# Kernel tuning notes

Hardware: AMD Instinct MI355X
Metric: run time of the kernel (lower is better)

The kernel has to match this reference:

```python
import jax, jax.numpy as jnp
import numpy as np

B, S, H, E, V = 16, 512, 1024, 256, 50257


def setup_inputs() -> dict:
    key = jax.random.key(0)
    ks = jax.random.split(key, 16)
    sc = 0.02
    return {
        "x": jax.random.randint(ks[0], (B, 1), 0, V),
        "dec_hs": jax.random.normal(ks[1], (1, B, H), jnp.float32),
        "enc_output": jax.random.normal(ks[2], (S, B, H), jnp.float32),
        "emb": jax.random.normal(ks[3], (V, E), jnp.float32) * sc,
        "w1_W": jax.random.normal(ks[4], (H, H), jnp.float32) * sc,
        "w1_b": jnp.zeros((H,), jnp.float32),
        "w2_W": jax.random.normal(ks[5], (H, H), jnp.float32) * sc,
        "w2_b": jnp.zeros((H,), jnp.float32),
        "va_W": jax.random.normal(ks[6], (1, H), jnp.float32) * sc,
        "va_b": jnp.zeros((1,), jnp.float32),
        "W_ih": jax.random.normal(ks[7], (3 * H, E + H), jnp.float32) * sc,
        "W_hh": jax.random.normal(ks[8], (3 * H, H), jnp.float32) * sc,
        "b_ih": jnp.zeros((3 * H,), jnp.float32),
        "b_hh": jnp.zeros((3 * H,), jnp.float32),
        "out_W": jax.random.normal(ks[9], (V, H), jnp.float32) * sc,
        "out_b": jnp.zeros((V,), jnp.float32),
    }


def reference(x, dec_hs, enc_output, emb, w1_W, w1_b, w2_W, w2_b, va_W, va_b,
              W_ih, W_hh, b_ih, b_hh, out_W, out_b):
    # --- Bahdanau attention ---
    # dec_hs: [1,B,H], enc_output: [S,B,H]
    dec_proj = dec_hs @ w1_W.T + w1_b           # [1,B,H]
    enc_proj = enc_output @ w2_W.T + w2_b       # [S,B,H]
    score = jnp.tanh(dec_proj + enc_proj) @ va_W.T + va_b  # [S,B,1]
    score = jnp.transpose(score, (1, 0, 2))     # [B,S,1]
    attn = jax.nn.softmax(score, axis=1)        # [B,S,1]
    context = jnp.sum(attn * jnp.transpose(enc_output, (1, 0, 2)), axis=1)  # [B,H]

    # --- embedding + concat (context first, as in torch.cat([ctx, emb])) ---
    e = emb[x[:, 0]]                            # [B,E]
    gru_in = jnp.concatenate([context, e], axis=-1)  # [B,H+E]

    # --- GRU single step; NOTE: original calls self.GRU(inp) without dec_hs,
    # so the initial hidden state is zeros (faithful to the source). ---
    h0 = jnp.zeros((gru_in.shape[0], w1_W.shape[0]), gru_in.dtype)  # [B,H]
    gi = gru_in @ W_ih.T + b_ih                 # [B,3H]
    gh = h0 @ W_hh.T + b_hh                     # [B,3H]
    i_r, i_z, i_n = jnp.split(gi, 3, axis=-1)
    h_r, h_z, h_n = jnp.split(gh, 3, axis=-1)
    r = jax.nn.sigmoid(i_r + h_r)
    z = jax.nn.sigmoid(i_z + h_z)
    n = jnp.tanh(i_n + r * h_n)
    h = (1.0 - z) * n + z * h0                  # [B,H]

    fc_out = h @ out_W.T + out_b                # [B,V]
    new_dec_hs = h[None]                        # [1,B,H]
    return fc_out, new_dec_hs, attn
```

## Files before the change

### kernel.cpp

```cpp
#include <hip/hip_runtime.h>
#include <hip/hip_bf16.h>

typedef unsigned short u16;
typedef __attribute__((ext_vector_type(4))) float f32x4;
typedef __attribute__((ext_vector_type(8))) __bf16 bf16x8;
typedef __attribute__((ext_vector_type(8))) unsigned short ushort8;

#define Bb 16
#define Ss 512
#define Hh 1024
#define Ee 256
#define Vv 50257
#define Mm 8192

#define WS_ENC_BF   0
#define WS_W2_BF    16777216
#define WS_DPW      18874368
#define WS_SCORE    18939904
#define WS_GRUIN    18972672
#define WS_GI       19054592

__device__ __forceinline__ u16 f2bf(float f) {
  unsigned u = __float_as_uint(f);
  return (u16)((u + 0x7FFFu + ((u >> 16) & 1u)) >> 16);
}

__device__ __forceinline__ void gl2lds16(const void* g, void* l) {
  __builtin_amdgcn_global_load_lds((__attribute__((address_space(1))) void*)g,
                                   (__attribute__((address_space(3))) void*)l,
                                   16, 0, 0);
}

__global__ __launch_bounds__(256) void k_cvt2(const float* __restrict__ enc, u16* __restrict__ encb,
                                              const float* __restrict__ w2, u16* __restrict__ w2b) {
  int i = blockIdx.x * 256 + threadIdx.x;
  const float* src; u16* dst; int j;
  if (i < 1048576) { src = enc; dst = encb; j = i; }
  else             { src = w2;  dst = w2b;  j = i - 1048576; }
  const float4* s4 = (const float4*)src;
  float4 a = s4[j * 2], c = s4[j * 2 + 1];
  ushort8 o;
  o[0] = f2bf(a.x); o[1] = f2bf(a.y); o[2] = f2bf(a.z); o[3] = f2bf(a.w);
  o[4] = f2bf(c.x); o[5] = f2bf(c.y); o[6] = f2bf(c.z); o[7] = f2bf(c.w);
  *(ushort8*)(dst + j * 8) = o;
}

__global__ __launch_bounds__(256) void k_prep(const float* __restrict__ dec_hs, const float* __restrict__ w1_W,
                                              const float* __restrict__ w1_b, const float* __restrict__ w2_b,
                                              const float* __restrict__ va_b, const int* __restrict__ x,
                                              const float* __restrict__ emb, float* __restrict__ dpw,
                                              float* __restrict__ score, float* __restrict__ gru_in) {
  const int n = blockIdx.x, t = threadIdx.x;
  float acc[16];
#pragma unroll
  for (int b = 0; b < 16; ++b) acc[b] = 0.f;
#pragma unroll
  for (int i = 0; i < 4; ++i) {
    int k = t + i * 256;
    float w = w1_W[n * Hh + k];
#pragma unroll
    for (int b = 0; b < 16; ++b) acc[b] = fmaf(w, dec_hs[b * Hh + k], acc[b]);
  }
#pragma unroll
  for (int m = 1; m < 64; m <<= 1)
#pragma unroll
    for (int b = 0; b < 16; ++b) acc[b] += __shfl_xor(acc[b], m, 64);
  __shared__ float red[4][16];
  int wave = t >> 6, lane = t & 63;
  if (lane == 0)
#pragma unroll
    for (int b = 0; b < 16; ++b) red[wave][b] = acc[b];
  __syncthreads();
  if (t < 16)
    dpw[t * Hh + n] = red[0][t] + red[1][t] + red[2][t] + red[3][t] + w1_b[n] + w2_b[n];
  int fid = n * 256 + t;
  if (fid < 16384) { int b = fid >> 10, k = fid & 1023; gru_in[b * 1280 + k] = 0.f; }
  int sid = fid - 16384;
  if (sid >= 0 && sid < Mm) score[sid] = va_b[0];
  int eid = fid - 24576;
  if (eid >= 0 && eid < 4096) { int b = eid >> 8, j = eid & 255; gru_in[b * 1280 + 1024 + j] = emb[x[b] * Ee + j]; }
}

__global__ __launch_bounds__(256) void k_gemm_score(const u16* __restrict__ A, const u16* __restrict__ Bm,
                                                    const float* __restrict__ dpw, const float* __restrict__ vaW,
                                                    float* __restrict__ score) {
  __shared__ __align__(16) u16 Al[4096];
  __shared__ __align__(16) u16 Bl[4096];
  const int tid = threadIdx.x;
  const int wave = tid >> 6, lane = tid & 63;
  const int quad = lane >> 4, l16 = lane & 15;
  const int m0 = blockIdx.x * 128, n0 = blockIdx.y * 128;
  const int wm = (wave & 1) * 64, wn = (wave >> 1) * 64;

  f32x4 acc[4][4];
#pragma unroll
  for (int i = 0; i < 4; ++i)
#pragma unroll
    for (int j = 0; j < 4; ++j) acc[i][j] = (f32x4){0.f, 0.f, 0.f, 0.f};

  const u16* gA = A + (m0 + (tid >> 2)) * 1024 + (tid & 3) * 8;
  const u16* gB = Bm + (n0 + (tid >> 2)) * 1024 + (tid & 3) * 8;
  u16* lA0 = &Al[(wave * 64) * 8];
  u16* lA1 = &Al[(256 + wave * 64) * 8];
  u16* lB0 = &Bl[(wave * 64) * 8];
  u16* lB1 = &Bl[(256 + wave * 64) * 8];

  for (int kt = 0; kt < 1024; kt += 32) {
    __syncthreads();
    gl2lds16(gA + kt, lA0);
    gl2lds16(gA + 64 * 1024 + kt, lA1);
    gl2lds16(gB + kt, lB0);
    gl2lds16(gB + 64 * 1024 + kt, lB1);
    __syncthreads();
    bf16x8 af[4], bfr[4];
#pragma unroll
    for (int i = 0; i < 4; ++i) {
      af[i]  = *(const bf16x8*)&Al[(wm + i * 16 + l16) * 32 + quad * 8];
      bfr[i] = *(const bf16x8*)&Bl[(wn + i * 16 + l16) * 32 + quad * 8];
    }
#pragma unroll
    for (int i = 0; i < 4; ++i)
#pragma unroll
      for (int j = 0; j < 4; ++j)
        acc[i][j] = __builtin_amdgcn_mfma_f32_16x16x32_bf16(af[i], bfr[j], acc[i][j], 0, 0, 0);
  }

  __syncthreads();
  float* dpw_t = (float*)Al;
  float* va_t  = (float*)Bl;
  for (int idx = tid; idx < 2048; idx += 256) {
    int b = idx >> 7, nn = idx & 127;
    dpw_t[idx] = dpw[b * Hh + n0 + nn];
  }
  if (tid < 128) va_t[tid] = vaW[n0 + tid];
  __syncthreads();

  float rs[4][4];
#pragma unroll
  for (int i = 0; i < 4; ++i)
#pragma unroll
    for (int r = 0; r < 4; ++r) rs[i][r] = 0.f;
#pragma unroll
  for (int i = 0; i < 4; ++i)
#pragma unroll
    for (int j = 0; j < 4; ++j) {
      int nn = wn + j * 16 + l16;
      float va = va_t[nn];
#pragma unroll
      for (int r = 0; r < 4; ++r) {
        float xv = acc[i][j][r] + dpw_t[(quad * 4 + r) * 128 + nn];
        rs[i][r] += tanhf(xv) * va;
      }
    }
#pragma unroll
  for (int i = 0; i < 4; ++i)
#pragma unroll
    for (int r = 0; r < 4; ++r) {
      float v = rs[i][r];
      v += __shfl_xor(v, 1, 64);
      v += __shfl_xor(v, 2, 64);
      v += __shfl_xor(v, 4, 64);
      v += __shfl_xor(v, 8, 64);
      if (l16 == 0) atomicAdd(&score[m0 + wm + i * 16 + quad * 4 + r], v);
    }
}

__global__ __launch_bounds__(256) void k_softmax(const float* __restrict__ score, float* __restrict__ attn) {
  const int b = blockIdx.x, t = threadIdx.x;
  __shared__ float red[256];
  float v0 = score[t * Bb + b];
  float v1 = score[(t + 256) * Bb + b];
  red[t] = fmaxf(v0, v1);
  __syncthreads();
  for (int s = 128; s > 0; s >>= 1) { if (t < s) red[t] = fmaxf(red[t], red[t + s]); __syncthreads(); }
  float mx = red[0];
  __syncthreads();
  float e0 = expf(v0 - mx), e1 = expf(v1 - mx);
  red[t] = e0 + e1;
  __syncthreads();
  for (int s = 128; s > 0; s >>= 1) { if (t < s) red[t] += red[t + s]; __syncthreads(); }
  float inv = 1.f / red[0];
  attn[b * Ss + t] = e0 * inv;
  attn[b * Ss + t + 256] = e1 * inv;
}

__global__ __launch_bounds__(256) void k_context(const float* __restrict__ attn, const float* __restrict__ enc,
                                                 float* __restrict__ gru_in) {
  const int b = blockIdx.x, sc = blockIdx.y, t = threadIdx.x;
  const int s0 = sc * 16;
  float acc[4] = {0.f, 0.f, 0.f, 0.f};
  for (int s = s0; s < s0 + 16; ++s) {
    float a = attn[b * Ss + s];
    const float* e = enc + (s * Bb + b) * Hh;
#pragma unroll
    for (int hh = 0; hh < 4; ++hh) acc[hh] = fmaf(a, e[t + hh * 256], acc[hh]);
  }
#pragma unroll
  for (int hh = 0; hh < 4; ++hh) atomicAdd(&gru_in[b * 1280 + t + hh * 256], acc[hh]);
}

__global__ __launch_bounds__(256) void k_gi(const float* __restrict__ W_ih, const float* __restrict__ gru_in,
                                            const float* __restrict__ b_ih, float* __restrict__ gi) {
  const int n = blockIdx.x, t = threadIdx.x;
  float acc[16];
#pragma unroll
  for (int b = 0; b < 16; ++b) acc[b] = 0.f;
#pragma unroll
  for (int i = 0; i < 5; ++i) {
    int k = t + i * 256;
    float w = W_ih[n * 1280 + k];
#pragma unroll
    for (int b = 0; b < 16; ++b) acc[b] = fmaf(w, gru_in[b * 1280 + k], acc[b]);
  }
#pragma unroll
  for (int m = 1; m < 64; m <<= 1)
#pragma unroll
    for (int b = 0; b < 16; ++b) acc[b] += __shfl_xor(acc[b], m, 64);
  __shared__ float red[4][16];
  int wave = t >> 6, lane = t & 63;
  if (lane == 0)
#pragma unroll
    for (int b = 0; b < 16; ++b) red[wave][b] = acc[b];
  __syncthreads();
  if (t < 16)
    gi[t * 3072 + n] = red[0][t] + red[1][t] + red[2][t] + red[3][t] + b_ih[n];
}

__global__ __launch_bounds__(256) void k_gates(const float* __restrict__ gi, const float* __restrict__ b_hh,
                                               float* __restrict__ h_out) {
  int idx = blockIdx.x * 256 + threadIdx.x;
  int b = idx >> 10, j = idx & 1023;
  float ir = gi[b * 3072 + j], iz = gi[b * 3072 + 1024 + j], in_ = gi[b * 3072 + 2048 + j];
  float r = 1.f / (1.f + expf(-(ir + b_hh[j])));
  float z = 1.f / (1.f + expf(-(iz + b_hh[1024 + j])));
  float n = tanhf(in_ + r * b_hh[2048 + j]);
  h_out[idx] = (1.f - z) * n;
}

__global__ __launch_bounds__(256) void k_fc(const float* __restrict__ out_W, const float* __restrict__ out_b,
                                            const float* __restrict__ h, float* __restrict__ fc) {
  __shared__ __align__(16) float tile[128 * 128];
  const int tid = threadIdx.x;
  const int wave = tid >> 6, lane = tid & 63;
  const int khalf = __builtin_amdgcn_readfirstlane(wave >> 1);
  const int row = (wave & 1) * 64 + lane;
  const int v0 = blockIdx.x * 128;

  float acc[16];
#pragma unroll
  for (int b = 0; b < 16; ++b) acc[b] = 0.f;

  for (int c = 0; c < 8; ++c) {
    __syncthreads();
#pragma unroll
    for (int i = 0; i < 16; ++i) {
      int r = wave * 32 + i * 2 + (lane >> 5);
      int gblk = (lane & 31) ^ (r & 7);
      int vrow = v0 + r;
      if (vrow > Vv - 1) vrow = Vv - 1;
      const float* g = out_W + (long)vrow * Hh + c * 128 + gblk * 4;
      float* l = tile + (wave * 32 + i * 2) * 128;
      gl2lds16(g, l);
    }
    __syncthreads();
    const float* hb = h + c * 128 + khalf * 64;
#pragma unroll
    for (int kk = 0; kk < 64; kk += 4) {
      int blk = khalf * 16 + (kk >> 2);
      int sblk = blk ^ (row & 7);
      float4 w = *(const float4*)&tile[row * 128 + sblk * 4];
#pragma unroll
      for (int b = 0; b < 16; ++b) {
        float4 hv = *(const float4*)&hb[b * Hh + kk];
        acc[b] = fmaf(w.x, hv.x, acc[b]);
        acc[b] = fmaf(w.y, hv.y, acc[b]);
        acc[b] = fmaf(w.z, hv.z, acc[b]);
        acc[b] = fmaf(w.w, hv.w, acc[b]);
      }
    }
  }

  __syncthreads();
  float* red = tile;
  if (khalf == 1) {
#pragma unroll
    for (int b = 0; b < 16; ++b) red[row * 16 + b] = acc[b];
  }
  __syncthreads();
  if (khalf == 0) {
    int v = v0 + row;
    if (v < Vv) {
      float ob = out_b[v];
#pragma unroll
      for (int b = 0; b < 16; ++b)
        fc[(long)b * Vv + v] = acc[b] + red[row * 16 + b] + ob;
    }
  }
}

extern "C" void kernel_launch(void* const* d_in, const int* in_sizes, int n_in,
                              void* d_out, int out_size, void* d_ws, size_t ws_size,
                              hipStream_t stream) {
  const int*   x       = (const int*)d_in[0];
  const float* dec_hs  = (const float*)d_in[1];
  const float* enc_out = (const float*)d_in[2];
  const float* emb     = (const float*)d_in[3];
  const float* w1_W    = (const float*)d_in[4];
  const float* w1_b    = (const float*)d_in[5];
  const float* w2_W    = (const float*)d_in[6];
  const float* w2_b    = (const float*)d_in[7];
  const float* va_W    = (const float*)d_in[8];
  const float* va_b    = (const float*)d_in[9];
  const float* W_ih    = (const float*)d_in[10];
  const float* b_ih    = (const float*)d_in[12];
  const float* b_hh    = (const float*)d_in[13];
  const float* out_W   = (const float*)d_in[14];
  const float* out_b   = (const float*)d_in[15];

  char* ws = (char*)d_ws;
  u16*   enc_bf = (u16*)(ws + WS_ENC_BF);
  u16*   w2_bf  = (u16*)(ws + WS_W2_BF);
  float* dpw    = (float*)(ws + WS_DPW);
  float* score  = (float*)(ws + WS_SCORE);
  float* gru_in = (float*)(ws + WS_GRUIN);
  float* gi     = (float*)(ws + WS_GI);

  float* fc       = (float*)d_out;
  float* h_out    = fc + (long)Bb * Vv;
  float* attn_out = h_out + Bb * Hh;

  k_cvt2<<<4608, 256, 0, stream>>>(enc_out, enc_bf, w2_W, w2_bf);
  k_prep<<<1024, 256, 0, stream>>>(dec_hs, w1_W, w1_b, w2_b, va_b, x, emb, dpw, score, gru_in);
  k_gemm_score<<<dim3(64, 8), 256, 0, stream>>>(enc_bf, w2_bf, dpw, va_W, score);
  k_softmax<<<16, 256, 0, stream>>>(score, attn_out);
  k_context<<<dim3(16, 32), 256, 0, stream>>>(attn_out, enc_out, gru_in);
  k_gi<<<3072, 256, 0, stream>>>(W_ih, gru_in, b_ih, gi);
  k_gates<<<64, 256, 0, stream>>>(gi, b_hh, h_out);
  k_fc<<<(Vv + 127) / 128, 256, 0, stream>>>(out_W, out_b, h_out, fc);
}
```

Measured before the change: 515.2 us.

## Use bf16 MFMA with split hi/lo hidden state for output projection

```diff
diff --git a/kernel.cpp b/kernel.cpp
--- a/kernel.cpp
+++ b/kernel.cpp
@@ -19,6 +19,8 @@
 #define WS_SCORE    18939904
 #define WS_GRUIN    18972672
 #define WS_GI       19054592
+#define WS_HA_HI    19251200
+#define WS_HA_LO    19283968
 
 __device__ __forceinline__ u16 f2bf(float f) {
   unsigned u = __float_as_uint(f);
@@ -227,73 +229,80 @@
 }
 
 __global__ __launch_bounds__(256) void k_gates(const float* __restrict__ gi, const float* __restrict__ b_hh,
-                                               float* __restrict__ h_out) {
+                                               float* __restrict__ h_out, u16* __restrict__ hA_hi,
+                                               u16* __restrict__ hA_lo) {
   int idx = blockIdx.x * 256 + threadIdx.x;
   int b = idx >> 10, j = idx & 1023;
   float ir = gi[b * 3072 + j], iz = gi[b * 3072 + 1024 + j], in_ = gi[b * 3072 + 2048 + j];
   float r = 1.f / (1.f + expf(-(ir + b_hh[j])));
   float z = 1.f / (1.f + expf(-(iz + b_hh[1024 + j])));
   float n = tanhf(in_ + r * b_hh[2048 + j]);
-  h_out[idx] = (1.f - z) * n;
+  float hv = (1.f - z) * n;
+  h_out[idx] = hv;
+  u16 hi = f2bf(hv);
+  float hi_f = __uint_as_float((unsigned)hi << 16);
+  u16 lo = f2bf(hv - hi_f);
+  int g = j >> 3, jj = j & 7;
+  hA_hi[g * 128 + b * 8 + jj] = hi;
+  hA_lo[g * 128 + b * 8 + jj] = lo;
 }
 
 __global__ __launch_bounds__(256) void k_fc(const float* __restrict__ out_W, const float* __restrict__ out_b,
-                                            const float* __restrict__ h, float* __restrict__ fc) {
+                                            const u16* __restrict__ hA_hi, const u16* __restrict__ hA_lo,
+                                            float* __restrict__ fc) {
   __shared__ __align__(16) float tile[128 * 128];
   const int tid = threadIdx.x;
   const int wave = tid >> 6, lane = tid & 63;
-  const int khalf = __builtin_amdgcn_readfirstlane(wave >> 1);
-  const int row = (wave & 1) * 64 + lane;
+  const int quad = lane >> 4, l16 = lane & 15;
   const int v0 = blockIdx.x * 128;
 
-  float acc[16];
-#pragma unroll
-  for (int b = 0; b < 16; ++b) acc[b] = 0.f;
+  f32x4 acc[2];
+  acc[0] = (f32x4){0.f, 0.f, 0.f, 0.f};
+  acc[1] = (f32x4){0.f, 0.f, 0.f, 0.f};
 
   for (int c = 0; c < 8; ++c) {
     __syncthreads();
 #pragma unroll
     for (int i = 0; i < 16; ++i) {
       int r = wave * 32 + i * 2 + (lane >> 5);
-      int gblk = (lane & 31) ^ (r & 7);
+      int gg = (lane & 31) ^ (r & 7);
       int vrow = v0 + r;
       if (vrow > Vv - 1) vrow = Vv - 1;
-      const float* g = out_W + (long)vrow * Hh + c * 128 + gblk * 4;
+      const float* g = out_W + (long)vrow * Hh + c * 128 + gg * 4;
       float* l = tile + (wave * 32 + i * 2) * 128;
       gl2lds16(g, l);
     }
     __syncthreads();
-    const float* hb = h + c * 128 + khalf * 64;
-#pragma unroll
-    for (int kk = 0; kk < 64; kk += 4) {
-      int blk = khalf * 16 + (kk >> 2);
-      int sblk = blk ^ (row & 7);
-      float4 w = *(const float4*)&tile[row * 128 + sblk * 4];
-#pragma unroll
-      for (int b = 0; b < 16; ++b) {
-        float4 hv = *(const float4*)&hb[b * Hh + kk];
-        acc[b] = fmaf(w.x, hv.x, acc[b]);
-        acc[b] = fmaf(w.y, hv.y, acc[b]);
-        acc[b] = fmaf(w.z, hv.z, acc[b]);
-        acc[b] = fmaf(w.w, hv.w, acc[b]);
+#pragma unroll
+    for (int s = 0; s < 4; ++s) {
+      int gbase = c * 16 + s * 4 + quad;
+      bf16x8 a_hi = *(const bf16x8*)(hA_hi + gbase * 128 + l16 * 8);
+      bf16x8 a_lo = *(const bf16x8*)(hA_lo + gbase * 128 + l16 * 8);
+#pragma unroll
+      for (int t = 0; t < 2; ++t) {
+        int vl = wave * 32 + t * 16 + l16;
+        int m0 = s * 8 + quad * 2;
+        int p0 = m0 ^ (vl & 7), p1 = (m0 + 1) ^ (vl & 7);
+        const float* rowp = tile + vl * 128;
+        f32x4 w0 = *(const f32x4*)(rowp + p0 * 4);
+        f32x4 w1 = *(const f32x4*)(rowp + p1 * 4);
+        union { ushort8 u; bf16x8 b; } bu;
+        bu.u[0] = f2bf(w0[0]); bu.u[1] = f2bf(w0[1]); bu.u[2] = f2bf(w0[2]); bu.u[3] = f2bf(w0[3]);
+        bu.u[4] = f2bf(w1[0]); bu.u[5] = f2bf(w1[1]); bu.u[6] = f2bf(w1[2]); bu.u[7] = f2bf(w1[3]);
+        acc[t] = __builtin_amdgcn_mfma_f32_16x16x32_bf16(a_hi, bu.b, acc[t], 0, 0, 0);
+        acc[t] = __builtin_amdgcn_mfma_f32_16x16x32_bf16(a_lo, bu.b, acc[t], 0, 0, 0);
       }
     }
   }
 
-  __syncthreads();
-  float* red = tile;
-  if (khalf == 1) {
-#pragma unroll
-    for (int b = 0; b < 16; ++b) red[row * 16 + b] = acc[b];
-  }
-  __syncthreads();
-  if (khalf == 0) {
-    int v = v0 + row;
+#pragma unroll
+  for (int t = 0; t < 2; ++t) {
+    int v = v0 + wave * 32 + t * 16 + l16;
     if (v < Vv) {
       float ob = out_b[v];
 #pragma unroll
-      for (int b = 0; b < 16; ++b)
-        fc[(long)b * Vv + v] = acc[b] + red[row * 16 + b] + ob;
+      for (int r = 0; r < 4; ++r)
+        fc[(long)(quad * 4 + r) * Vv + v] = acc[t][r] + ob;
     }
   }
 }
@@ -324,6 +333,8 @@
   float* score  = (float*)(ws + WS_SCORE);
   float* gru_in = (float*)(ws + WS_GRUIN);
   float* gi     = (float*)(ws + WS_GI);
+  u16*   hA_hi  = (u16*)(ws + WS_HA_HI);
+  u16*   hA_lo  = (u16*)(ws + WS_HA_LO);
 
   float* fc       = (float*)d_out;
   float* h_out    = fc + (long)Bb * Vv;
@@ -335,6 +346,6 @@
   k_softmax<<<16, 256, 0, stream>>>(score, attn_out);
   k_context<<<dim3(16, 32), 256, 0, stream>>>(attn_out, enc_out, gru_in);
   k_gi<<<3072, 256, 0, stream>>>(W_ih, gru_in, b_ih, gi);
-  k_gates<<<64, 256, 0, stream>>>(gi, b_hh, h_out);
-  k_fc<<<(Vv + 127) / 128, 256, 0, stream>>>(out_W, out_b, h_out, fc);
-}
+  k_gates<<<64, 256, 0, stream>>>(gi, b_hh, h_out, hA_hi, hA_lo);
+  k_fc<<<(Vv + 127) / 128, 256, 0, stream>>>(out_W, out_b, hA_hi, hA_lo, fc);
+}
```

After: 450.2 us. 1.14x faster.
